# Kernel optimization log

Measured on AMD Instinct MI355X. Metric: run time of the kernel, lower is better.

## Reference

```python
import jax, jax.numpy as jnp
import numpy as np

H = 1024        # hidden_size
E = 3           # num_smear experts
DI = 1280       # int(1.25 * H), GRU inner dim (expansion_factor=1.25)
EPS = 1e-6


def setup_inputs() -> dict:
    key = jax.random.key(0)
    ks = jax.random.split(key, 5)
    B, S = 4, 4096
    s = 0.02
    return {
        "inputs": jax.random.normal(ks[0], (B, S, H), jnp.float32),
        "norm_weight": jnp.ones((H,), jnp.float32),
        "router_w": jax.random.normal(ks[1], (H, E), jnp.float32) * s,
        "router_b": jnp.zeros((E,), jnp.float32),
        "w_in": jax.random.normal(ks[2], (E, H, 2 * DI), jnp.float32) * s,
        "b_in": jnp.zeros((E, 2 * DI), jnp.float32),
        "w_out": jax.random.normal(ks[3], (E, DI, H), jnp.float32) * s,
        "b_out": jnp.zeros((E, H), jnp.float32),
    }


def _g(x):
    # minGRU candidate activation: x + 0.5 for x >= 0, sigmoid(x) otherwise
    return jnp.where(x >= 0, x + 0.5, jax.nn.sigmoid(x))


def reference(inputs, norm_weight, router_w, router_b, w_in, b_in, w_out, b_out):
    B, S, _ = inputs.shape
    # RMSNorm
    x = inputs * jax.lax.rsqrt(jnp.mean(inputs * inputs, axis=-1, keepdims=True) + EPS)
    x = x * norm_weight

    # SMEAR routing: softmax over experts from mean-pooled tokens, per sample
    pooled = x.mean(axis=1)                                   # [B, H]
    probs = jax.nn.softmax(pooled @ router_w + router_b, -1)  # [B, E]

    # Soft-merge expert parameters per sample
    Wi = jnp.einsum('be,edh->bdh', probs, w_in)    # [B, H, 2*DI]
    bi = jnp.einsum('be,eh->bh', probs, b_in)      # [B, 2*DI]
    Wo = jnp.einsum('be,edh->bdh', probs, w_out)   # [B, DI, H]
    bo = jnp.einsum('be,eh->bh', probs, b_out)     # [B, H]

    # GRU (minGRU) input projection
    zh = jnp.einsum('bsd,bdh->bsh', x, Wi) + bi[:, None, :]   # [B, S, 2*DI]
    hid, gate = jnp.split(zh, 2, axis=-1)
    z = jax.nn.sigmoid(gate)   # update gate [B, S, DI]
    ht = _g(hid)               # candidate    [B, S, DI]

    def step(h, zt_ht):
        z_t, ht_t = zt_ht
        h = (1.0 - z_t) * h + z_t * ht_t
        return h, h

    h0 = jnp.zeros((B, DI), x.dtype)
    _, hs = jax.lax.scan(step, h0, (z.swapaxes(0, 1), ht.swapaxes(0, 1)))
    hs = hs.swapaxes(0, 1)     # [B, S, DI]

    out = jnp.einsum('bsh,bhd->bsd', hs, Wo) + bo[:, None, :]  # proj_out
    out = out + inputs                                          # residual (dropout=0, eval)
    new_state = hs[:, -1]                                       # [B, DI]
    aux_loss = jnp.zeros((), inputs.dtype)
    return out, new_state, aux_loss
```

## Files before the change

kernel.cpp:

```cpp
#include <hip/hip_runtime.h>
#include <hip/hip_bf16.h>

#define B_  4
#define S_  4096
#define H_  1024
#define DI_ 1280
#define DI2_ 2560
#define E_  3
#define NC_ 64
#define CL_ 64
#define EPS_ 1e-6f

typedef unsigned short ushort_t;
typedef __attribute__((ext_vector_type(8))) __bf16 bf16x8;
typedef __attribute__((ext_vector_type(4))) float f32x4;

__device__ inline ushort_t f2bf(float f) {
    union { float f; unsigned u; } v; v.f = f;
    unsigned r = v.u + 0x7fffu + ((v.u >> 16) & 1u);
    return (ushort_t)(r >> 16);
}
__device__ inline float bf2f(ushort_t s) {
    union { unsigned u; float f; } v; v.u = ((unsigned)s) << 16;
    return v.f;
}
__device__ inline float sigmoidf_(float x) { return 1.0f / (1.0f + __expf(-x)); }

__device__ inline void gld16(const void* g, void* l) {
    __builtin_amdgcn_global_load_lds(
        (const __attribute__((address_space(1))) void*)g,
        (__attribute__((address_space(3))) void*)l, 16, 0, 0);
}

__global__ __launch_bounds__(256) void rmsnorm_kernel(
    const float* __restrict__ in, const float* __restrict__ nw,
    ushort_t* __restrict__ xbf, float* __restrict__ partial)
{
    int g = blockIdx.x, b = blockIdx.y;
    int tid = threadIdx.x, lane = tid & 63, w = tid >> 6;
    int s0 = g * 16;
    const float4* inb = (const float4*)(in + ((size_t)b * S_ + s0) * H_);
    float4 rows[16];
    float ss[16];
#pragma unroll
    for (int r = 0; r < 16; r++) {
        float4 v = inb[(size_t)r * (H_ / 4) + tid];
        rows[r] = v;
        ss[r] = v.x * v.x + v.y * v.y + v.z * v.z + v.w * v.w;
    }
#pragma unroll
    for (int r = 0; r < 16; r++) {
        float s = ss[r];
        s += __shfl_down(s, 32); s += __shfl_down(s, 16); s += __shfl_down(s, 8);
        s += __shfl_down(s, 4);  s += __shfl_down(s, 2);  s += __shfl_down(s, 1);
        ss[r] = s;
    }
    __shared__ float red[16][4];
    __shared__ float scl[16];
    if (lane == 0) {
#pragma unroll
        for (int r = 0; r < 16; r++) red[r][w] = ss[r];
    }
    __syncthreads();
    if (tid < 16) {
        float t = red[tid][0] + red[tid][1] + red[tid][2] + red[tid][3];
        scl[tid] = rsqrtf(t * (1.0f / H_) + EPS_);
    }
    __syncthreads();
    float4 nw4 = ((const float4*)nw)[tid];
    float4 pacc = {0.f, 0.f, 0.f, 0.f};
    ushort_t* xrow = xbf + ((size_t)b * S_ + s0) * H_;
#pragma unroll
    for (int r = 0; r < 16; r++) {
        float sc = scl[r];
        float4 v = rows[r];
        v.x = v.x * sc * nw4.x; v.y = v.y * sc * nw4.y;
        v.z = v.z * sc * nw4.z; v.w = v.w * sc * nw4.w;
        ushort4 u; u.x = f2bf(v.x); u.y = f2bf(v.y); u.z = f2bf(v.z); u.w = f2bf(v.w);
        *(ushort4*)(xrow + (size_t)r * H_ + tid * 4) = u;
        pacc.x += v.x; pacc.y += v.y; pacc.z += v.z; pacc.w += v.w;
    }
    float4* pp = (float4*)(partial + ((size_t)(b * 256 + g)) * H_);
    pp[tid] = pacc;
}

__global__ __launch_bounds__(256) void reduce_kernel(
    const float* __restrict__ partial, float* __restrict__ partial2)
{
    int b = blockIdx.x, j = blockIdx.y, tid = threadIdx.x;
    float4 acc = {0.f, 0.f, 0.f, 0.f};
    const float4* pp = (const float4*)partial;
    for (int g = j * 32; g < j * 32 + 32; g++) {
        float4 v = pp[((size_t)(b * 256 + g)) * (H_ / 4) + tid];
        acc.x += v.x; acc.y += v.y; acc.z += v.z; acc.w += v.w;
    }
    ((float4*)partial2)[((size_t)(b * 8 + j)) * (H_ / 4) + tid] = acc;
}

__global__ __launch_bounds__(256) void router_kernel(
    const float* __restrict__ partial2, const float* __restrict__ rw,
    const float* __restrict__ rb, const float* __restrict__ b_in,
    const float* __restrict__ b_out, float* __restrict__ probs,
    float* __restrict__ bi, float* __restrict__ bo, float* __restrict__ aux)
{
    int b = blockIdx.x;
    int tid = threadIdx.x, lane = tid & 63, w = tid >> 6;
    float4 acc = {0.f, 0.f, 0.f, 0.f};
    const float4* pp = (const float4*)partial2;
    for (int g = 0; g < 8; g++) {
        float4 v = pp[((size_t)(b * 8 + g)) * (H_ / 4) + tid];
        acc.x += v.x; acc.y += v.y; acc.z += v.z; acc.w += v.w;
    }
    const float inv_s = 1.0f / (float)S_;
    float a4[4] = {acc.x * inv_s, acc.y * inv_s, acc.z * inv_s, acc.w * inv_s};
    float le[3] = {0.f, 0.f, 0.f};
    int h0 = tid * 4;
#pragma unroll
    for (int j = 0; j < 4; j++) {
        float p = a4[j];
        le[0] += p * rw[(size_t)(h0 + j) * 3 + 0];
        le[1] += p * rw[(size_t)(h0 + j) * 3 + 1];
        le[2] += p * rw[(size_t)(h0 + j) * 3 + 2];
    }
#pragma unroll
    for (int e = 0; e < 3; e++) {
        float s = le[e];
        s += __shfl_down(s, 32); s += __shfl_down(s, 16); s += __shfl_down(s, 8);
        s += __shfl_down(s, 4);  s += __shfl_down(s, 2);  s += __shfl_down(s, 1);
        le[e] = s;
    }
    __shared__ float red[4][3];
    __shared__ float pr[3];
    if (lane == 0) { red[w][0] = le[0]; red[w][1] = le[1]; red[w][2] = le[2]; }
    __syncthreads();
    if (tid == 0) {
        float l0 = red[0][0] + red[1][0] + red[2][0] + red[3][0] + rb[0];
        float l1 = red[0][1] + red[1][1] + red[2][1] + red[3][1] + rb[1];
        float l2 = red[0][2] + red[1][2] + red[2][2] + red[3][2] + rb[2];
        float m = fmaxf(l0, fmaxf(l1, l2));
        float e0 = __expf(l0 - m), e1 = __expf(l1 - m), e2 = __expf(l2 - m);
        float inv = 1.0f / (e0 + e1 + e2);
        pr[0] = e0 * inv; pr[1] = e1 * inv; pr[2] = e2 * inv;
    }
    __syncthreads();
    if (tid < 3) probs[b * 3 + tid] = pr[tid];
    float p0 = pr[0], p1 = pr[1], p2 = pr[2];
    for (int n = tid; n < DI2_; n += 256) {
        int d = n >> 1;
        int src = (n & 1) ? (DI_ + d) : d;
        bi[(size_t)b * DI2_ + n] = p0 * b_in[src] + p1 * b_in[DI2_ + src] + p2 * b_in[2 * DI2_ + src];
    }
    for (int n = tid; n < H_; n += 256)
        bo[(size_t)b * H_ + n] = p0 * b_out[n] + p1 * b_out[H_ + n] + p2 * b_out[2 * H_ + n];
    if (b == 0 && tid == 0) *aux = 0.0f;
}

__global__ __launch_bounds__(256) void mix_kernel(
    const float* __restrict__ wsrc, const float* __restrict__ probs,
    ushort_t* __restrict__ dst, int K, int N)
{
    int kt = blockIdx.x, nt = blockIdx.y, b = blockIdx.z;
    float p0 = probs[b * 3 + 0], p1 = probs[b * 3 + 1], p2 = probs[b * 3 + 2];
    __shared__ float T[64][65];
    int tid = threadIdx.x;
    int c = tid & 63, rr = tid >> 6;
    const float* w0 = wsrc;
    const float* w1 = wsrc + (size_t)K * N;
    const float* w2 = wsrc + 2 * (size_t)K * N;
    int k0 = kt * 64, n0 = nt * 64;
#pragma unroll
    for (int pass = 0; pass < 16; pass++) {
        int r = pass * 4 + rr;
        size_t idx = (size_t)(k0 + r) * N + n0 + c;
        T[r][c] = p0 * w0[idx] + p1 * w1[idx] + p2 * w2[idx];
    }
    __syncthreads();
    ushort_t* db = dst + (size_t)b * N * K;
#pragma unroll
    for (int pass = 0; pass < 16; pass++) {
        int j = pass * 4 + rr;
        db[(size_t)(n0 + j) * K + k0 + c] = f2bf(T[c][j]);
    }
}

__global__ __launch_bounds__(256) void mix_in_kernel(
    const float* __restrict__ wsrc, const float* __restrict__ probs,
    ushort_t* __restrict__ dst)
{
    int kt = blockIdx.x, dt = blockIdx.y, b = blockIdx.z;
    float p0 = probs[b * 3 + 0], p1 = probs[b * 3 + 1], p2 = probs[b * 3 + 2];
    __shared__ float Th[64][33];
    __shared__ float Tg[64][33];
    int tid = threadIdx.x;
    int k0 = kt * 64, d0 = dt * 32;
    const float* w0 = wsrc;
    const float* w1 = wsrc + (size_t)H_ * DI2_;
    const float* w2 = wsrc + 2 * (size_t)H_ * DI2_;
    {
        int c = tid & 31, rr = tid >> 5;
#pragma unroll
        for (int pass = 0; pass < 8; pass++) {
            int r = pass * 8 + rr;
            size_t ih = (size_t)(k0 + r) * DI2_ + d0 + c;
            size_t ig = ih + DI_;
            Th[r][c] = p0 * w0[ih] + p1 * w1[ih] + p2 * w2[ih];
            Tg[r][c] = p0 * w0[ig] + p1 * w1[ig] + p2 * w2[ig];
        }
    }
    __syncthreads();
    ushort_t* db = dst + (size_t)b * DI2_ * H_;
    int n0i = d0 * 2;
    int c = tid & 63, rr = tid >> 6;
#pragma unroll
    for (int pass = 0; pass < 16; pass++) {
        int jj = pass * 4 + rr;
        int d = jj >> 1;
        float v = (jj & 1) ? Tg[c][d] : Th[c][d];
        db[(size_t)(n0i + jj) * H_ + k0 + c] = f2bf(v);
    }
}

template <int MODE>
__global__ __launch_bounds__(256, 2) void gemm_bt(
    const ushort_t* __restrict__ Aall, const ushort_t* __restrict__ Btall,
    int M, int N, int K,
    const float* __restrict__ biasAll,
    const float* __restrict__ resAll, float* __restrict__ outAll,
    ushort_t* __restrict__ zhAll)
{
    __shared__ ushort_t As[2 * 128 * 32];
    __shared__ ushort_t Bs[2 * 128 * 32];
    int b = blockIdx.z;
    const ushort_t* A = Aall + (size_t)b * M * K;
    const ushort_t* Bt = Btall + (size_t)b * N * K;
    int tid = threadIdx.x, lane = tid & 63, w = tid >> 6;

    int num_n = N >> 7;
    const int GROUP = 4;
    int gsz = GROUP * num_n;
    int gid = blockIdx.x / gsz, rem = blockIdx.x % gsz;
    int mt = gid * GROUP + (rem & (GROUP - 1));
    int nt = rem >> 2;
    int mblk = mt * 128, nblk = nt * 128;

    int srow = lane >> 2;
    int sblk = (lane & 3) ^ ((srow >> 1) & 3);
    int scol = sblk * 8;
    const ushort_t* ga0 = A + (size_t)(mblk + (w * 2 + 0) * 16 + srow) * K + scol;
    const ushort_t* ga1 = A + (size_t)(mblk + (w * 2 + 1) * 16 + srow) * K + scol;
    const ushort_t* gb0 = Bt + (size_t)(nblk + (w * 2 + 0) * 16 + srow) * K + scol;
    const ushort_t* gb1 = Bt + (size_t)(nblk + (w * 2 + 1) * 16 + srow) * K + scol;
    ushort_t* la0 = &As[(w * 2 + 0) * 512 + lane * 8];
    ushort_t* la1 = &As[(w * 2 + 1) * 512 + lane * 8];
    ushort_t* lb0 = &Bs[(w * 2 + 0) * 512 + lane * 8];
    ushort_t* lb1 = &Bs[(w * 2 + 1) * 512 + lane * 8];

    f32x4 acc[4][4] = {};
    int wy = w & 1, wx = w >> 1;
    int q = lane >> 4;
    int ml = lane & 15;
    int rblk = (q ^ ((ml >> 1) & 3)) * 8;
    int aoff0 = wy * 2048 + ml * 32 + rblk;
    int boff0 = wx * 2048 + ml * 32 + rblk;

    for (int k0 = 0; k0 < K; k0 += 64) {
        gld16(ga0, la0);       gld16(ga1, la1);
        gld16(gb0, lb0);       gld16(gb1, lb1);
        gld16(ga0 + 32, la0 + 4096); gld16(ga1 + 32, la1 + 4096);
        gld16(gb0 + 32, lb0 + 4096); gld16(gb1 + 32, lb1 + 4096);
        ga0 += 64; ga1 += 64; gb0 += 64; gb1 += 64;
        __syncthreads();
#pragma unroll
        for (int p = 0; p < 2; p++) {
            bf16x8 af[4], bfr[4];
#pragma unroll
            for (int i = 0; i < 4; i++) af[i] = *(const bf16x8*)&As[p * 4096 + aoff0 + i * 512];
#pragma unroll
            for (int i = 0; i < 4; i++) bfr[i] = *(const bf16x8*)&Bs[p * 4096 + boff0 + i * 512];
#pragma unroll
            for (int mi = 0; mi < 4; mi++)
#pragma unroll
                for (int ni = 0; ni < 4; ni++)
                    acc[mi][ni] = __builtin_amdgcn_mfma_f32_16x16x32_bf16(bfr[ni], af[mi], acc[mi][ni], 0, 0, 0);
        }
        __syncthreads();
    }

    int nq = nblk + wx * 64 + q * 4;
    const float* bias = biasAll + (size_t)b * N;
    if (MODE == 0) {
        ushort_t* dst = zhAll + (size_t)b * (size_t)M * N;
#pragma unroll
        for (int mi = 0; mi < 4; mi++) {
            int m = mblk + wy * 64 + mi * 16 + ml;
            ushort_t* drow = dst + (size_t)m * N;
#pragma unroll
            for (int ni = 0; ni < 4; ni++) {
                int n0 = nq + ni * 16;
                float4 bv = *(const float4*)&bias[n0];
                f32x4 a = acc[mi][ni];
                float h0 = a[0] + bv.x, z0 = a[1] + bv.y;
                float h1 = a[2] + bv.z, z1 = a[3] + bv.w;
                float ht0 = (h0 >= 0.f) ? (h0 + 0.5f) : sigmoidf_(h0);
                float ht1 = (h1 >= 0.f) ? (h1 + 0.5f) : sigmoidf_(h1);
                float zz0 = sigmoidf_(z0), zz1 = sigmoidf_(z1);
                ushort4 u; u.x = f2bf(ht0); u.y = f2bf(zz0); u.z = f2bf(ht1); u.w = f2bf(zz1);
                *(ushort4*)&drow[n0] = u;
            }
        }
    } else {
        const float* resb = resAll + (size_t)b * (size_t)M * N;
        float* outp = outAll + (size_t)b * (size_t)M * N;
#pragma unroll
        for (int mi = 0; mi < 4; mi++) {
            int m = mblk + wy * 64 + mi * 16 + ml;
            const float* rrow = resb + (size_t)m * N;
            float* orow = outp + (size_t)m * N;
#pragma unroll
            for (int ni = 0; ni < 4; ni++) {
                int n0 = nq + ni * 16;
                float4 bv = *(const float4*)&bias[n0];
                float4 rv = *(const float4*)&rrow[n0];
                f32x4 a = acc[mi][ni];
                float4 o;
                o.x = a[0] + bv.x + rv.x; o.y = a[1] + bv.y + rv.y;
                o.z = a[2] + bv.z + rv.z; o.w = a[3] + bv.w + rv.w;
                *(float4*)&orow[n0] = o;
            }
        }
    }
}

__global__ __launch_bounds__(320) void scan_phase1(
    const ushort_t* __restrict__ zh, float* __restrict__ cA, float* __restrict__ cB)
{
    int d0 = threadIdx.x * 4;
    int c = blockIdx.x, b = blockIdx.y;
    const ushort_t* base = zh + ((size_t)b * S_ + (size_t)c * CL_) * DI2_ + d0 * 2;
    float A[4] = {1.f, 1.f, 1.f, 1.f};
    float Bc[4] = {0.f, 0.f, 0.f, 0.f};
    for (int t = 0; t < CL_; t++) {
        uint4 u = *(const uint4*)(base + (size_t)t * DI2_);
        unsigned uu[4] = {u.x, u.y, u.z, u.w};
#pragma unroll
        for (int j = 0; j < 4; j++) {
            float ht = bf2f((ushort_t)(uu[j] & 0xffff));
            float z  = bf2f((ushort_t)(uu[j] >> 16));
            float a = 1.f - z;
            A[j] *= a;
            Bc[j] = a * Bc[j] + z * ht;
        }
    }
    size_t o = ((size_t)b * NC_ + c) * DI_ + d0;
    float4 av; av.x = A[0]; av.y = A[1]; av.z = A[2]; av.w = A[3];
    float4 bv; bv.x = Bc[0]; bv.y = Bc[1]; bv.z = Bc[2]; bv.w = Bc[3];
    *(float4*)&cA[o] = av;
    *(float4*)&cB[o] = bv;
}

__global__ __launch_bounds__(256) void scan_phase2(
    const float* __restrict__ cA, const float* __restrict__ cB,
    float* __restrict__ h0buf, float* __restrict__ ns)
{
    int g = blockIdx.x * 256 + threadIdx.x;
    int b = g / (DI_ / 4), dq = g % (DI_ / 4);
    int d0 = dq * 4;
    float4 h = {0.f, 0.f, 0.f, 0.f};
    for (int c = 0; c < NC_; c++) {
        size_t o = ((size_t)b * NC_ + c) * DI_ + d0;
        *(float4*)&h0buf[o] = h;
        float4 a = *(const float4*)&cA[o];
        float4 bb = *(const float4*)&cB[o];
        h.x = a.x * h.x + bb.x; h.y = a.y * h.y + bb.y;
        h.z = a.z * h.z + bb.z; h.w = a.w * h.w + bb.w;
    }
    *(float4*)&ns[(size_t)b * DI_ + d0] = h;
}

__global__ __launch_bounds__(320) void scan_phase3(
    const ushort_t* __restrict__ zh, const float* __restrict__ h0buf,
    ushort_t* __restrict__ hs)
{
    int d0 = threadIdx.x * 4;
    int c = blockIdx.x, b = blockIdx.y;
    const ushort_t* base = zh + ((size_t)b * S_ + (size_t)c * CL_) * DI2_ + d0 * 2;
    ushort_t* hbase = hs + ((size_t)b * S_ + (size_t)c * CL_) * DI_ + d0;
    float4 h0 = *(const float4*)&h0buf[((size_t)b * NC_ + c) * DI_ + d0];
    float h[4] = {h0.x, h0.y, h0.z, h0.w};
    for (int t = 0; t < CL_; t++) {
        uint4 u = *(const uint4*)(base + (size_t)t * DI2_);
        unsigned uu[4] = {u.x, u.y, u.z, u.w};
        ushort4 o;
#pragma unroll
        for (int j = 0; j < 4; j++) {
            float ht = bf2f((ushort_t)(uu[j] & 0xffff));
            float z  = bf2f((ushort_t)(uu[j] >> 16));
            h[j] = (1.f - z) * h[j] + z * ht;
        }
        o.x = f2bf(h[0]); o.y = f2bf(h[1]); o.z = f2bf(h[2]); o.w = f2bf(h[3]);
        *(ushort4*)(hbase + (size_t)t * DI_) = o;
    }
}

extern "C" void kernel_launch(void* const* d_in, const int* in_sizes, int n_in,
                              void* d_out, int out_size, void* d_ws, size_t ws_size,
                              hipStream_t stream)
{
    const float* in    = (const float*)d_in[0];
    const float* nw    = (const float*)d_in[1];
    const float* rw    = (const float*)d_in[2];
    const float* rb    = (const float*)d_in[3];
    const float* w_in  = (const float*)d_in[4];
    const float* b_in  = (const float*)d_in[5];
    const float* w_out = (const float*)d_in[6];
    const float* b_out = (const float*)d_in[7];
    float* out = (float*)d_out;

    char* ws = (char*)d_ws;
    size_t off = 0;
    auto nxt = [&](size_t bytes) -> void* {
        void* p = ws + off;
        off += (bytes + 255) & ~(size_t)255;
        return p;
    };
    ushort_t* xbf    = (ushort_t*)nxt((size_t)B_ * S_ * H_ * 2);
    ushort_t* wi_t   = (ushort_t*)nxt((size_t)B_ * DI2_ * H_ * 2);
    ushort_t* wo_t   = (ushort_t*)nxt((size_t)B_ * H_ * DI_ * 2);
    ushort_t* zhbuf  = (ushort_t*)nxt((size_t)B_ * S_ * DI2_ * 2);
    ushort_t* hsbuf  = (ushort_t*)nxt((size_t)B_ * S_ * DI_ * 2);
    float* partial   = (float*)nxt((size_t)B_ * 256 * H_ * 4);
    float* partial2  = (float*)nxt((size_t)B_ * 8 * H_ * 4);
    float* probs     = (float*)nxt((size_t)B_ * 3 * 4);
    float* bi        = (float*)nxt((size_t)B_ * DI2_ * 4);
    float* bo        = (float*)nxt((size_t)B_ * H_ * 4);
    float* cA        = (float*)nxt((size_t)B_ * NC_ * DI_ * 4);
    float* cB        = (float*)nxt((size_t)B_ * NC_ * DI_ * 4);
    float* h0buf     = (float*)nxt((size_t)B_ * NC_ * DI_ * 4);

    float* ns  = out + (size_t)B_ * S_ * H_;
    float* aux = ns + (size_t)B_ * DI_;

    rmsnorm_kernel<<<dim3(S_ / 16, B_), 256, 0, stream>>>(in, nw, xbf, partial);
    reduce_kernel<<<dim3(B_, 8), 256, 0, stream>>>(partial, partial2);
    router_kernel<<<dim3(B_), 256, 0, stream>>>(partial2, rw, rb, b_in, b_out, probs, bi, bo, aux);
    mix_in_kernel<<<dim3(H_ / 64, DI_ / 32, B_), 256, 0, stream>>>(w_in, probs, wi_t);
    mix_kernel<<<dim3(DI_ / 64, H_ / 64, B_), 256, 0, stream>>>(w_out, probs, wo_t, DI_, H_);
    gemm_bt<0><<<dim3((S_ / 128) * (DI2_ / 128), 1, B_), 256, 0, stream>>>(
        xbf, wi_t, S_, DI2_, H_, bi, nullptr, nullptr, zhbuf);
    scan_phase1<<<dim3(NC_, B_), 320, 0, stream>>>(zhbuf, cA, cB);
    scan_phase2<<<dim3(5), 256, 0, stream>>>(cA, cB, h0buf, ns);
    scan_phase3<<<dim3(NC_, B_), 320, 0, stream>>>(zhbuf, h0buf, hsbuf);
    gemm_bt<1><<<dim3((S_ / 128) * (H_ / 128), 1, B_), 256, 0, stream>>>(
        hsbuf, wo_t, S_, H_, DI_, bo, in, out, nullptr);
    (void)in_sizes; (void)n_in; (void)out_size; (void)ws_size;
}
```

Before: 428.1 us.

## Load expert weights once for all batches; finer scan chunks and wider phase2

Measured after the change: 436.1 us. Within noise of the previous version (+1.9%).

```diff
diff --git a/kernel.cpp b/kernel.cpp
--- a/kernel.cpp
+++ b/kernel.cpp
@@ -7,8 +7,8 @@
 #define DI_ 1280
 #define DI2_ 2560
 #define E_  3
-#define NC_ 64
-#define CL_ 64
+#define NC_ 128
+#define CL_ 32
 #define EPS_ 1e-6f
 
 typedef unsigned short ushort_t;
@@ -159,27 +159,31 @@
     const float* __restrict__ wsrc, const float* __restrict__ probs,
     ushort_t* __restrict__ dst, int K, int N)
 {
-    int kt = blockIdx.x, nt = blockIdx.y, b = blockIdx.z;
-    float p0 = probs[b * 3 + 0], p1 = probs[b * 3 + 1], p2 = probs[b * 3 + 2];
-    __shared__ float T[64][65];
+    int kt = blockIdx.x, nt = blockIdx.y;
+    __shared__ float T[3][64][65];
     int tid = threadIdx.x;
     int c = tid & 63, rr = tid >> 6;
-    const float* w0 = wsrc;
-    const float* w1 = wsrc + (size_t)K * N;
-    const float* w2 = wsrc + 2 * (size_t)K * N;
     int k0 = kt * 64, n0 = nt * 64;
 #pragma unroll
-    for (int pass = 0; pass < 16; pass++) {
-        int r = pass * 4 + rr;
-        size_t idx = (size_t)(k0 + r) * N + n0 + c;
-        T[r][c] = p0 * w0[idx] + p1 * w1[idx] + p2 * w2[idx];
-    }
-    __syncthreads();
-    ushort_t* db = dst + (size_t)b * N * K;
-#pragma unroll
-    for (int pass = 0; pass < 16; pass++) {
-        int j = pass * 4 + rr;
-        db[(size_t)(n0 + j) * K + k0 + c] = f2bf(T[c][j]);
+    for (int e = 0; e < 3; e++) {
+        const float* we = wsrc + (size_t)e * K * N;
+#pragma unroll
+        for (int pass = 0; pass < 16; pass++) {
+            int r = pass * 4 + rr;
+            T[e][r][c] = we[(size_t)(k0 + r) * N + n0 + c];
+        }
+    }
+    __syncthreads();
+#pragma unroll
+    for (int b = 0; b < B_; b++) {
+        float p0 = probs[b * 3 + 0], p1 = probs[b * 3 + 1], p2 = probs[b * 3 + 2];
+        ushort_t* db = dst + (size_t)b * N * K;
+#pragma unroll
+        for (int pass = 0; pass < 16; pass++) {
+            int j = pass * 4 + rr;
+            float v = p0 * T[0][c][j] + p1 * T[1][c][j] + p2 * T[2][c][j];
+            db[(size_t)(n0 + j) * K + k0 + c] = f2bf(v);
+        }
     }
 }
 
@@ -187,36 +191,41 @@
     const float* __restrict__ wsrc, const float* __restrict__ probs,
     ushort_t* __restrict__ dst)
 {
-    int kt = blockIdx.x, dt = blockIdx.y, b = blockIdx.z;
-    float p0 = probs[b * 3 + 0], p1 = probs[b * 3 + 1], p2 = probs[b * 3 + 2];
-    __shared__ float Th[64][33];
-    __shared__ float Tg[64][33];
+    int kt = blockIdx.x, dt = blockIdx.y;
+    __shared__ float Th[3][64][33];
+    __shared__ float Tg[3][64][33];
     int tid = threadIdx.x;
     int k0 = kt * 64, d0 = dt * 32;
-    const float* w0 = wsrc;
-    const float* w1 = wsrc + (size_t)H_ * DI2_;
-    const float* w2 = wsrc + 2 * (size_t)H_ * DI2_;
     {
         int c = tid & 31, rr = tid >> 5;
 #pragma unroll
-        for (int pass = 0; pass < 8; pass++) {
-            int r = pass * 8 + rr;
-            size_t ih = (size_t)(k0 + r) * DI2_ + d0 + c;
-            size_t ig = ih + DI_;
-            Th[r][c] = p0 * w0[ih] + p1 * w1[ih] + p2 * w2[ih];
-            Tg[r][c] = p0 * w0[ig] + p1 * w1[ig] + p2 * w2[ig];
-        }
-    }
-    __syncthreads();
-    ushort_t* db = dst + (size_t)b * DI2_ * H_;
+        for (int e = 0; e < 3; e++) {
+            const float* we = wsrc + (size_t)e * H_ * DI2_;
+#pragma unroll
+            for (int pass = 0; pass < 8; pass++) {
+                int r = pass * 8 + rr;
+                size_t ih = (size_t)(k0 + r) * DI2_ + d0 + c;
+                Th[e][r][c] = we[ih];
+                Tg[e][r][c] = we[ih + DI_];
+            }
+        }
+    }
+    __syncthreads();
     int n0i = d0 * 2;
     int c = tid & 63, rr = tid >> 6;
 #pragma unroll
-    for (int pass = 0; pass < 16; pass++) {
-        int jj = pass * 4 + rr;
-        int d = jj >> 1;
-        float v = (jj & 1) ? Tg[c][d] : Th[c][d];
-        db[(size_t)(n0i + jj) * H_ + k0 + c] = f2bf(v);
+    for (int b = 0; b < B_; b++) {
+        float p0 = probs[b * 3 + 0], p1 = probs[b * 3 + 1], p2 = probs[b * 3 + 2];
+        ushort_t* db = dst + (size_t)b * DI2_ * H_;
+#pragma unroll
+        for (int pass = 0; pass < 16; pass++) {
+            int jj = pass * 4 + rr;
+            int d = jj >> 1;
+            float v = (jj & 1)
+                ? (p0 * Tg[0][c][d] + p1 * Tg[1][c][d] + p2 * Tg[2][c][d])
+                : (p0 * Th[0][c][d] + p1 * Th[1][c][d] + p2 * Th[2][c][d]);
+            db[(size_t)(n0i + jj) * H_ + k0 + c] = f2bf(v);
+        }
     }
 }
 
@@ -363,18 +372,14 @@
     float* __restrict__ h0buf, float* __restrict__ ns)
 {
     int g = blockIdx.x * 256 + threadIdx.x;
-    int b = g / (DI_ / 4), dq = g % (DI_ / 4);
-    int d0 = dq * 4;
-    float4 h = {0.f, 0.f, 0.f, 0.f};
+    int b = g / DI_, d = g % DI_;
+    float h = 0.f;
     for (int c = 0; c < NC_; c++) {
-        size_t o = ((size_t)b * NC_ + c) * DI_ + d0;
-        *(float4*)&h0buf[o] = h;
-        float4 a = *(const float4*)&cA[o];
-        float4 bb = *(const float4*)&cB[o];
-        h.x = a.x * h.x + bb.x; h.y = a.y * h.y + bb.y;
-        h.z = a.z * h.z + bb.z; h.w = a.w * h.w + bb.w;
-    }
-    *(float4*)&ns[(size_t)b * DI_ + d0] = h;
+        size_t o = ((size_t)b * NC_ + c) * DI_ + d;
+        h0buf[o] = h;
+        h = cA[o] * h + cB[o];
+    }
+    ns[(size_t)b * DI_ + d] = h;
 }
 
 __global__ __launch_bounds__(320) void scan_phase3(
@@ -443,12 +448,12 @@
     rmsnorm_kernel<<<dim3(S_ / 16, B_), 256, 0, stream>>>(in, nw, xbf, partial);
     reduce_kernel<<<dim3(B_, 8), 256, 0, stream>>>(partial, partial2);
     router_kernel<<<dim3(B_), 256, 0, stream>>>(partial2, rw, rb, b_in, b_out, probs, bi, bo, aux);
-    mix_in_kernel<<<dim3(H_ / 64, DI_ / 32, B_), 256, 0, stream>>>(w_in, probs, wi_t);
-    mix_kernel<<<dim3(DI_ / 64, H_ / 64, B_), 256, 0, stream>>>(w_out, probs, wo_t, DI_, H_);
+    mix_in_kernel<<<dim3(H_ / 64, DI_ / 32), 256, 0, stream>>>(w_in, probs, wi_t);
+    mix_kernel<<<dim3(DI_ / 64, H_ / 64), 256, 0, stream>>>(w_out, probs, wo_t, DI_, H_);
     gemm_bt<0><<<dim3((S_ / 128) * (DI2_ / 128), 1, B_), 256, 0, stream>>>(
         xbf, wi_t, S_, DI2_, H_, bi, nullptr, nullptr, zhbuf);
     scan_phase1<<<dim3(NC_, B_), 320, 0, stream>>>(zhbuf, cA, cB);
-    scan_phase2<<<dim3(5), 256, 0, stream>>>(cA, cB, h0buf, ns);
+    scan_phase2<<<dim3((B_ * DI_) / 256), 256, 0, stream>>>(cA, cB, h0buf, ns);
     scan_phase3<<<dim3(NC_, B_), 320, 0, stream>>>(zhbuf, h0buf, hsbuf);
     gemm_bt<1><<<dim3((S_ / 128) * (H_ / 128), 1, B_), 256, 0, stream>>>(
         hsbuf, wo_t, S_, H_, DI_, bo, in, out, nullptr);
```
